# Performance work log

Hardware: AMD Instinct MI355X
Metric: run time of the kernel (lower is better)

The kernel has to match this reference:

```python
import jax, jax.numpy as jnp
import numpy as np

N0, N1, N2 = 819200, 81920, 8192
E1, E2 = 819200, 81920
DIN, DH, DOUT = 128, 256, 128


def setup_inputs() -> dict:
    key = jax.random.key(0)
    ks = jax.random.split(key, 12)
    inp = {
        "x": jax.random.normal(ks[0], (N0, DIN), dtype=jnp.float32),
        "src1": jax.random.randint(ks[1], (E1,), 0, N0, dtype=jnp.int32),
        "dst1": jax.random.randint(ks[2], (E1,), 0, N1, dtype=jnp.int32),
        "src2": jax.random.randint(ks[3], (E2,), 0, N1, dtype=jnp.int32),
        "dst2": jax.random.randint(ks[4], (E2,), 0, N2, dtype=jnp.int32),
        "n1": N1,
        "n2": N2,
        # SAGEConv layer 1 params (lin_l has bias, lin_r no bias, PyG default)
        "w1l": jax.random.normal(ks[5], (DIN, DH), dtype=jnp.float32) / np.sqrt(DIN),
        "b1": jnp.zeros((DH,), dtype=jnp.float32),
        "w1r": jax.random.normal(ks[6], (DIN, DH), dtype=jnp.float32) / np.sqrt(DIN),
        # SAGEConv layer 2 params
        "w2l": jax.random.normal(ks[7], (DH, DOUT), dtype=jnp.float32) / np.sqrt(DH),
        "b2": jnp.zeros((DOUT,), dtype=jnp.float32),
        "w2r": jax.random.normal(ks[8], (DH, DOUT), dtype=jnp.float32) / np.sqrt(DH),
    }
    return inp


def _sage_conv(x_src, x_dst, src, dst, n_dst, wl, bl, wr):
    # mean aggregation of neighbor (source) features into destinations
    msg = x_src[src]                                            # [E, d]
    agg = jax.ops.segment_sum(msg, dst, num_segments=n_dst)     # [n_dst, d]
    cnt = jax.ops.segment_sum(jnp.ones((dst.shape[0],), msg.dtype), dst,
                              num_segments=n_dst)               # [n_dst]
    mean = agg / jnp.maximum(cnt, 1.0)[:, None]
    return mean @ wl + bl + x_dst @ wr


def reference(x, src1, dst1, src2, dst2, n1, n2, w1l, b1, w1r, w2l, b2, w2r):
    # layer 1 (eval mode: dropout is a no-op)
    h = _sage_conv(x, x[:n1], src1, dst1, n1, w1l, b1, w1r)     # [n1, DH]
    h = jax.nn.relu(h)
    # layer 2
    out = _sage_conv(h, h[:n2], src2, dst2, n2, w2l, b2, w2r)   # [n2, DOUT]
    return out
```

## Files before the change

### kernel.cpp

```cpp
#include <hip/hip_runtime.h>

constexpr int cN0 = 819200, cN1 = 81920, cN2 = 8192;
constexpr int cE1 = 819200, cE2 = 81920;
constexpr int cDIN = 128, cDH = 256, cDOUT = 128;
constexpr int cNOFF = cN1 + cN2;

typedef __attribute__((ext_vector_type(8))) short bf16x8;
typedef __attribute__((ext_vector_type(4))) float f32x4;
typedef __attribute__((ext_vector_type(8))) unsigned short u16x8;

__device__ __forceinline__ unsigned short f2bf(float f) {
    unsigned u = __builtin_bit_cast(unsigned, f);
    u += 0x7FFF + ((u >> 16) & 1);
    return (unsigned short)(u >> 16);
}
__device__ __forceinline__ float bf2f(unsigned short s) {
    unsigned u = ((unsigned)s) << 16;
    return __builtin_bit_cast(float, u);
}

__global__ __launch_bounds__(256) void setup_k(
    int* __restrict__ offs,
    const float* __restrict__ w1l, const float* __restrict__ w1r,
    const float* __restrict__ w2l, const float* __restrict__ w2r,
    unsigned short* __restrict__ W1c, unsigned short* __restrict__ W2c)
{
    int id = blockIdx.x * 256 + threadIdx.x;
    if (id < cNOFF) { offs[id] = 0; return; }
    int t = id - cNOFF;
    if (t < 256 * 256) {
        int n = t >> 8, k = t & 255;
        float v = (k < 128) ? w1l[k * 256 + n] : w1r[(k - 128) * 256 + n];
        W1c[n * 256 + k] = f2bf(v);
    } else {
        t -= 256 * 256;
        if (t < 128 * 512) {
            int n = t >> 9, k = t & 511;
            float v = (k < 256) ? w2l[k * 128 + n] : w2r[(k - 256) * 128 + n];
            W2c[n * 512 + k] = f2bf(v);
        }
    }
}

__global__ __launch_bounds__(256) void hist_k(
    const int* __restrict__ dst1, const int* __restrict__ dst2,
    int* __restrict__ offs)
{
    int e = blockIdx.x * 256 + threadIdx.x;
    if (e < cE1) atomicAdd(&offs[dst1[e]], 1);
    else {
        int e2 = e - cE1;
        if (e2 < cE2) atomicAdd(&offs[cN1 + dst2[e2]], 1);
    }
}

__global__ __launch_bounds__(1024) void partial_k(
    const int* __restrict__ a, int* __restrict__ part)
{
    const int tid = threadIdx.x, lane = tid & 63, wid = tid >> 6;
    int v = a[blockIdx.x * 1024 + tid];
    #pragma unroll
    for (int off = 32; off; off >>= 1) v += __shfl_xor(v, off);
    __shared__ int ws[16];
    if (lane == 0) ws[wid] = v;
    __syncthreads();
    if (tid == 0) {
        int s = 0;
        #pragma unroll
        for (int i = 0; i < 16; ++i) s += ws[i];
        part[blockIdx.x] = s;
    }
}

__global__ __launch_bounds__(128) void scanp_k(int* __restrict__ part)
{
    const int tid = threadIdx.x, lane = tid & 63, wid = tid >> 6;
    int v = (tid < 88) ? part[tid] : 0;
    int incl = v;
    #pragma unroll
    for (int off = 1; off < 64; off <<= 1) {
        int t = __shfl_up(incl, off, 64);
        if (lane >= off) incl += t;
    }
    __shared__ int w0;
    if (wid == 0 && lane == 63) w0 = incl;
    __syncthreads();
    int pre = wid ? w0 : 0;
    if (tid < 88) part[tid] = pre + incl - v;
}

__global__ __launch_bounds__(1024) void final_k(
    int* __restrict__ a, const int* __restrict__ part)
{
    const int tid = threadIdx.x, lane = tid & 63, wid = tid >> 6;
    const int g = blockIdx.x * 1024 + tid;
    int v = a[g];
    int incl = v;
    #pragma unroll
    for (int off = 1; off < 64; off <<= 1) {
        int t = __shfl_up(incl, off, 64);
        if (lane >= off) incl += t;
    }
    __shared__ int ws[16];
    if (lane == 63) ws[wid] = incl;
    __syncthreads();
    int pre = 0;
    #pragma unroll
    for (int i = 0; i < 16; ++i) if (i < wid) pre += ws[i];
    int r = part[blockIdx.x] + pre + incl - v;
    if (g >= cN1) r -= cE1;
    a[g] = r;
}

__global__ __launch_bounds__(256) void build_k(
    const int* __restrict__ src1, const int* __restrict__ dst1,
    const int* __restrict__ src2, const int* __restrict__ dst2,
    int* __restrict__ offs, int* __restrict__ eidx1, int* __restrict__ eidx2)
{
    int e = blockIdx.x * 256 + threadIdx.x;
    if (e < cE1) {
        int p = atomicAdd(&offs[dst1[e]], 1);
        eidx1[p] = src1[e];
    } else {
        int e2 = e - cE1;
        if (e2 < cE2) {
            int p = atomicAdd(&offs[cN1 + dst2[e2]], 1);
            eidx2[p] = src2[e2];
        }
    }
}

__global__ __launch_bounds__(256) void agg1_k(
    const float* __restrict__ x, const int* __restrict__ cursor,
    const int* __restrict__ eidx, unsigned short* __restrict__ mean1)
{
    const int row = blockIdx.x * 4 + (threadIdx.x >> 6);
    const int lane = threadIdx.x & 63;
    const int g = lane >> 4, li = lane & 15;
    const int start = row ? cursor[row - 1] : 0;
    const int end = cursor[row];
    float acc[8] = {};
    for (int e = start + g; e < end; e += 4) {
        const int s = eidx[e];
        const float4* p = reinterpret_cast<const float4*>(x + (size_t)s * cDIN + li * 8);
        float4 a = p[0], b = p[1];
        acc[0] += a.x; acc[1] += a.y; acc[2] += a.z; acc[3] += a.w;
        acc[4] += b.x; acc[5] += b.y; acc[6] += b.z; acc[7] += b.w;
    }
    #pragma unroll
    for (int i = 0; i < 8; ++i) {
        acc[i] += __shfl_xor(acc[i], 16);
        acc[i] += __shfl_xor(acc[i], 32);
    }
    if (g == 0) {
        const float inv = 1.0f / fmaxf((float)(end - start), 1.0f);
        u16x8 o;
        #pragma unroll
        for (int i = 0; i < 8; ++i) o[i] = f2bf(acc[i] * inv);
        *reinterpret_cast<u16x8*>(mean1 + (size_t)row * cDIN + li * 8) = o;
    }
}

__global__ __launch_bounds__(256) void agg2_k(
    const unsigned short* __restrict__ h, const int* __restrict__ cursor,
    const int* __restrict__ eidx, unsigned short* __restrict__ mean2)
{
    const int row = blockIdx.x * 4 + (threadIdx.x >> 6);
    const int lane = threadIdx.x & 63;
    const int g = lane >> 4, li = lane & 15;
    const int start = row ? cursor[row - 1] : 0;
    const int end = cursor[row];
    float acc[16] = {};
    for (int e = start + g; e < end; e += 4) {
        const int s = eidx[e];
        const u16x8* p = reinterpret_cast<const u16x8*>(h + (size_t)s * cDH + li * 16);
        u16x8 a = p[0], b = p[1];
        #pragma unroll
        for (int i = 0; i < 8; ++i) { acc[i] += bf2f(a[i]); acc[8 + i] += bf2f(b[i]); }
    }
    #pragma unroll
    for (int i = 0; i < 16; ++i) {
        acc[i] += __shfl_xor(acc[i], 16);
        acc[i] += __shfl_xor(acc[i], 32);
    }
    if (g == 0) {
        const float inv = 1.0f / fmaxf((float)(end - start), 1.0f);
        u16x8 o0, o1;
        #pragma unroll
        for (int i = 0; i < 8; ++i) { o0[i] = f2bf(acc[i] * inv); o1[i] = f2bf(acc[8 + i] * inv); }
        u16x8* q = reinterpret_cast<u16x8*>(mean2 + (size_t)row * cDH + li * 16);
        q[0] = o0; q[1] = o1;
    }
}

template<int K, int N, int TM, bool RIGHT_F32, bool L1MODE>
__global__ __launch_bounds__(256) void mfma_gemm_k(
    const unsigned short* __restrict__ Aleft, const void* __restrict__ Aright,
    const unsigned short* __restrict__ Bt, const float* __restrict__ bias,
    unsigned short* __restrict__ hout, float* __restrict__ fout)
{
    constexpr int KL = K / 2;
    constexpr int LD = 40;
    constexpr int WR = 4;
    constexpr int WC = (TM == 128) ? 4 : 2;
    __shared__ unsigned short As[TM * LD];
    __shared__ unsigned short Bs[128 * LD];

    const int tid = threadIdx.x;
    const int l = tid & 63, w = tid >> 6;
    const int q = l >> 4, r16 = l & 15;
    const int wr0 = (TM == 128) ? (w >> 1) * 64 : 0;
    const int wc0 = (TM == 128) ? (w & 1) * 64 : w * 32;
    const int n0 = blockIdx.x * 128, row0 = blockIdx.y * TM;

    const f32x4 zero = {0.f, 0.f, 0.f, 0.f};
    f32x4 acc[WR][WC];
    #pragma unroll
    for (int m = 0; m < WR; ++m)
        #pragma unroll
        for (int n = 0; n < WC; ++n) acc[m][n] = zero;

    for (int k0 = 0; k0 < K; k0 += 32) {
        const bool left = (k0 < KL);
        __syncthreads();
        #pragma unroll
        for (int c = 0; c < (TM * 4) / 256; ++c) {
            int z = tid + c * 256;
            int r = z >> 2, o16 = z & 3;
            bf16x8 av;
            if (left) {
                av = *reinterpret_cast<const bf16x8*>(Aleft + (size_t)(row0 + r) * KL + k0 + o16 * 8);
            } else if (RIGHT_F32) {
                const float* p = (const float*)Aright + (size_t)(row0 + r) * KL + (k0 - KL) + o16 * 8;
                float4 u = *reinterpret_cast<const float4*>(p);
                float4 v = *reinterpret_cast<const float4*>(p + 4);
                av[0] = (short)f2bf(u.x); av[1] = (short)f2bf(u.y);
                av[2] = (short)f2bf(u.z); av[3] = (short)f2bf(u.w);
                av[4] = (short)f2bf(v.x); av[5] = (short)f2bf(v.y);
                av[6] = (short)f2bf(v.z); av[7] = (short)f2bf(v.w);
            } else {
                av = *reinterpret_cast<const bf16x8*>((const unsigned short*)Aright + (size_t)(row0 + r) * KL + (k0 - KL) + o16 * 8);
            }
            *reinterpret_cast<bf16x8*>(As + r * LD + o16 * 8) = av;
        }
        #pragma unroll
        for (int c = 0; c < 2; ++c) {
            int z = tid + c * 256;
            int r = z >> 2, o16 = z & 3;
            bf16x8 bv = *reinterpret_cast<const bf16x8*>(Bt + (size_t)(n0 + r) * K + k0 + o16 * 8);
            *reinterpret_cast<bf16x8*>(Bs + r * LD + o16 * 8) = bv;
        }
        __syncthreads();
        bf16x8 af[WR], bg[WC];
        #pragma unroll
        for (int m = 0; m < WR; ++m)
            af[m] = *reinterpret_cast<const bf16x8*>(As + (wr0 + 16 * m + r16) * LD + q * 8);
        #pragma unroll
        for (int n = 0; n < WC; ++n)
            bg[n] = *reinterpret_cast<const bf16x8*>(Bs + (wc0 + 16 * n + r16) * LD + q * 8);
        #pragma unroll
        for (int m = 0; m < WR; ++m)
            #pragma unroll
            for (int n = 0; n < WC; ++n)
                acc[m][n] = __builtin_amdgcn_mfma_f32_16x16x32_bf16(af[m], bg[n], acc[m][n], 0, 0, 0);
    }

    #pragma unroll
    for (int n = 0; n < WC; ++n) {
        const int col = n0 + wc0 + 16 * n + r16;
        const float bv = bias[col];
        #pragma unroll
        for (int m = 0; m < WR; ++m) {
            #pragma unroll
            for (int j = 0; j < 4; ++j) {
                const int row = row0 + wr0 + 16 * m + 4 * q + j;
                float v = acc[m][n][j] + bv;
                if (L1MODE) {
                    hout[(size_t)row * N + col] = f2bf(fmaxf(v, 0.f));
                } else {
                    fout[(size_t)row * N + col] = v;
                }
            }
        }
    }
}

extern "C" void kernel_launch(void* const* d_in, const int* in_sizes, int n_in,
                              void* d_out, int out_size, void* d_ws, size_t ws_size,
                              hipStream_t stream)
{
    const float* x    = (const float*)d_in[0];
    const int*   src1 = (const int*)d_in[1];
    const int*   dst1 = (const int*)d_in[2];
    const int*   src2 = (const int*)d_in[3];
    const int*   dst2 = (const int*)d_in[4];
    const float* w1l  = (const float*)d_in[7];
    const float* b1   = (const float*)d_in[8];
    const float* w1r  = (const float*)d_in[9];
    const float* w2l  = (const float*)d_in[10];
    const float* b2   = (const float*)d_in[11];
    const float* w2r  = (const float*)d_in[12];
    float* out = (float*)d_out;

    unsigned short* mean1 = (unsigned short*)d_ws;
    unsigned short* h     = mean1 + (size_t)cN1 * cDIN;
    unsigned short* mean2 = h + (size_t)cN1 * cDH;
    unsigned short* W1c   = mean2 + (size_t)cN2 * cDH;
    unsigned short* W2c   = W1c + 256 * 256;
    int* offs  = (int*)(W2c + 128 * 512);
    int* eidx1 = offs + cNOFF;
    int* eidx2 = eidx1 + cE1;
    int* part  = eidx2 + cE2;

    {
        int total = cNOFF + 256 * 256 + 128 * 512;
        setup_k<<<(total + 255) / 256, 256, 0, stream>>>(offs, w1l, w1r, w2l, w2r, W1c, W2c);
    }
    hist_k<<<(cE1 + cE2) / 256, 256, 0, stream>>>(dst1, dst2, offs);
    partial_k<<<cNOFF / 1024, 1024, 0, stream>>>(offs, part);
    scanp_k<<<1, 128, 0, stream>>>(part);
    final_k<<<cNOFF / 1024, 1024, 0, stream>>>(offs, part);
    build_k<<<(cE1 + cE2) / 256, 256, 0, stream>>>(src1, dst1, src2, dst2, offs, eidx1, eidx2);

    agg1_k<<<cN1 / 4, 256, 0, stream>>>(x, offs, eidx1, mean1);

    mfma_gemm_k<256, 256, 128, true, true><<<dim3(2, cN1 / 128), 256, 0, stream>>>(
        mean1, (const void*)x, W1c, b1, h, nullptr);

    agg2_k<<<cN2 / 4, 256, 0, stream>>>(h, offs + cN1, eidx2, mean2);

    mfma_gemm_k<512, 128, 64, false, false><<<dim3(1, cN2 / 64), 256, 0, stream>>>(
        mean2, (const void*)h, W2c, b2, nullptr, out);
}
```

Baseline: 240.3 us.

## Fuse CSR build into one cooperative kernel and use direct-to-LDS loads in GEMM1

```diff
diff --git a/kernel.cpp b/kernel.cpp
--- a/kernel.cpp
+++ b/kernel.cpp
@@ -1,9 +1,13 @@
 #include <hip/hip_runtime.h>
+#include <hip/hip_cooperative_groups.h>
+
+namespace cg = cooperative_groups;
 
 constexpr int cN0 = 819200, cN1 = 81920, cN2 = 8192;
 constexpr int cE1 = 819200, cE2 = 81920;
 constexpr int cDIN = 128, cDH = 256, cDOUT = 128;
 constexpr int cNOFF = cN1 + cN2;
+constexpr int cNBLK = 352;
 
 typedef __attribute__((ext_vector_type(8))) short bf16x8;
 typedef __attribute__((ext_vector_type(4))) float f32x4;
@@ -19,113 +23,126 @@
     return __builtin_bit_cast(float, u);
 }
 
-__global__ __launch_bounds__(256) void setup_k(
-    int* __restrict__ offs,
+#define GLOAD_LDS16(g, l) __builtin_amdgcn_global_load_lds(               \
+    (const __attribute__((address_space(1))) void*)(g),                   \
+    (__attribute__((address_space(3))) void*)(l), 16, 0, 0)
+
+__global__ __launch_bounds__(256) void csr_coop_k(
+    int* __restrict__ offs, int* __restrict__ part,
+    const int* __restrict__ dst1, const int* __restrict__ dst2,
+    const int* __restrict__ src1, const int* __restrict__ src2,
+    int* __restrict__ eidx1, int* __restrict__ eidx2,
+    const float* __restrict__ x, unsigned short* __restrict__ xb,
     const float* __restrict__ w1l, const float* __restrict__ w1r,
     const float* __restrict__ w2l, const float* __restrict__ w2r,
     unsigned short* __restrict__ W1c, unsigned short* __restrict__ W2c)
 {
-    int id = blockIdx.x * 256 + threadIdx.x;
-    if (id < cNOFF) { offs[id] = 0; return; }
-    int t = id - cNOFF;
-    if (t < 256 * 256) {
-        int n = t >> 8, k = t & 255;
-        float v = (k < 128) ? w1l[k * 256 + n] : w1r[(k - 128) * 256 + n];
-        W1c[n * 256 + k] = f2bf(v);
-    } else {
-        t -= 256 * 256;
-        if (t < 128 * 512) {
-            int n = t >> 9, k = t & 511;
+    cg::grid_group grid = cg::this_grid();
+    const int tid = threadIdx.x, bid = blockIdx.x;
+    const int lane = tid & 63, wid = tid >> 6;
+    const int gtid = bid * 256 + tid;
+    __shared__ int ws4[4];
+    __shared__ int carry;
+
+    offs[gtid] = 0;
+    __threadfence();
+    grid.sync();
+
+    for (int e = gtid; e < cE1 + cE2; e += cNOFF) {
+        if (e < cE1) atomicAdd(&offs[dst1[e]], 1);
+        else atomicAdd(&offs[cN1 + dst2[e - cE1]], 1);
+    }
+    __threadfence();
+    grid.sync();
+
+    {
+        int v = offs[gtid];
+        #pragma unroll
+        for (int off = 32; off; off >>= 1) v += __shfl_xor(v, off);
+        if (lane == 0) ws4[wid] = v;
+        __syncthreads();
+        if (tid == 0) part[bid] = ws4[0] + ws4[1] + ws4[2] + ws4[3];
+    }
+    __threadfence();
+    grid.sync();
+
+    if (bid == 0) {
+        if (tid == 0) carry = 0;
+        __syncthreads();
+        for (int base = 0; base < cNBLK; base += 256) {
+            const int i = base + tid;
+            int v = (i < cNBLK) ? part[i] : 0;
+            int incl = v;
+            #pragma unroll
+            for (int off = 1; off < 64; off <<= 1) {
+                int t = __shfl_up(incl, off, 64);
+                if (lane >= off) incl += t;
+            }
+            if (lane == 63) ws4[wid] = incl;
+            __syncthreads();
+            int wpre = 0;
+            #pragma unroll
+            for (int w = 0; w < 3; ++w) if (w < wid) wpre += ws4[w];
+            int c = carry;
+            if (i < cNBLK) part[i] = c + wpre + incl - v;
+            __syncthreads();
+            if (tid == 255) carry = c + wpre + incl;
+            __syncthreads();
+        }
+        __threadfence();
+    }
+    grid.sync();
+
+    {
+        int v = offs[gtid];
+        int incl = v;
+        #pragma unroll
+        for (int off = 1; off < 64; off <<= 1) {
+            int t = __shfl_up(incl, off, 64);
+            if (lane >= off) incl += t;
+        }
+        if (lane == 63) ws4[wid] = incl;
+        __syncthreads();
+        int pre = 0;
+        #pragma unroll
+        for (int w = 0; w < 3; ++w) if (w < wid) pre += ws4[w];
+        int r = part[bid] + pre + incl - v;
+        if (gtid >= cN1) r -= cE1;
+        offs[gtid] = r;
+    }
+    __threadfence();
+    grid.sync();
+
+    for (int e = gtid; e < cE1 + cE2; e += cNOFF) {
+        if (e < cE1) {
+            int p = atomicAdd(&offs[dst1[e]], 1);
+            eidx1[p] = src1[e];
+        } else {
+            int e2 = e - cE1;
+            int p = atomicAdd(&offs[cN1 + dst2[e2]], 1);
+            eidx2[p] = src2[e2];
+        }
+    }
+
+    for (int i = gtid; i < cN1 * cDIN / 8; i += cNOFF) {
+        const float* p = x + (size_t)i * 8;
+        float4 a = *reinterpret_cast<const float4*>(p);
+        float4 b = *reinterpret_cast<const float4*>(p + 4);
+        u16x8 o;
+        o[0] = f2bf(a.x); o[1] = f2bf(a.y); o[2] = f2bf(a.z); o[3] = f2bf(a.w);
+        o[4] = f2bf(b.x); o[5] = f2bf(b.y); o[6] = f2bf(b.z); o[7] = f2bf(b.w);
+        reinterpret_cast<u16x8*>(xb)[i] = o;
+    }
+    for (int t = gtid; t < 256 * 256 + 128 * 512; t += cNOFF) {
+        if (t < 256 * 256) {
+            int n = t >> 8, k = t & 255;
+            float v = (k < 128) ? w1l[k * 256 + n] : w1r[(k - 128) * 256 + n];
+            W1c[n * 256 + k] = f2bf(v);
+        } else {
+            int t2 = t - 256 * 256;
+            int n = t2 >> 9, k = t2 & 511;
             float v = (k < 256) ? w2l[k * 128 + n] : w2r[(k - 256) * 128 + n];
             W2c[n * 512 + k] = f2bf(v);
-        }
-    }
-}
-
-__global__ __launch_bounds__(256) void hist_k(
-    const int* __restrict__ dst1, const int* __restrict__ dst2,
-    int* __restrict__ offs)
-{
-    int e = blockIdx.x * 256 + threadIdx.x;
-    if (e < cE1) atomicAdd(&offs[dst1[e]], 1);
-    else {
-        int e2 = e - cE1;
-        if (e2 < cE2) atomicAdd(&offs[cN1 + dst2[e2]], 1);
-    }
-}
-
-__global__ __launch_bounds__(1024) void partial_k(
-    const int* __restrict__ a, int* __restrict__ part)
-{
-    const int tid = threadIdx.x, lane = tid & 63, wid = tid >> 6;
-    int v = a[blockIdx.x * 1024 + tid];
-    #pragma unroll
-    for (int off = 32; off; off >>= 1) v += __shfl_xor(v, off);
-    __shared__ int ws[16];
-    if (lane == 0) ws[wid] = v;
-    __syncthreads();
-    if (tid == 0) {
-        int s = 0;
-        #pragma unroll
-        for (int i = 0; i < 16; ++i) s += ws[i];
-        part[blockIdx.x] = s;
-    }
-}
-
-__global__ __launch_bounds__(128) void scanp_k(int* __restrict__ part)
-{
-    const int tid = threadIdx.x, lane = tid & 63, wid = tid >> 6;
-    int v = (tid < 88) ? part[tid] : 0;
-    int incl = v;
-    #pragma unroll
-    for (int off = 1; off < 64; off <<= 1) {
-        int t = __shfl_up(incl, off, 64);
-        if (lane >= off) incl += t;
-    }
-    __shared__ int w0;
-    if (wid == 0 && lane == 63) w0 = incl;
-    __syncthreads();
-    int pre = wid ? w0 : 0;
-    if (tid < 88) part[tid] = pre + incl - v;
-}
-
-__global__ __launch_bounds__(1024) void final_k(
-    int* __restrict__ a, const int* __restrict__ part)
-{
-    const int tid = threadIdx.x, lane = tid & 63, wid = tid >> 6;
-    const int g = blockIdx.x * 1024 + tid;
-    int v = a[g];
-    int incl = v;
-    #pragma unroll
-    for (int off = 1; off < 64; off <<= 1) {
-        int t = __shfl_up(incl, off, 64);
-        if (lane >= off) incl += t;
-    }
-    __shared__ int ws[16];
-    if (lane == 63) ws[wid] = incl;
-    __syncthreads();
-    int pre = 0;
-    #pragma unroll
-    for (int i = 0; i < 16; ++i) if (i < wid) pre += ws[i];
-    int r = part[blockIdx.x] + pre + incl - v;
-    if (g >= cN1) r -= cE1;
-    a[g] = r;
-}
-
-__global__ __launch_bounds__(256) void build_k(
-    const int* __restrict__ src1, const int* __restrict__ dst1,
-    const int* __restrict__ src2, const int* __restrict__ dst2,
-    int* __restrict__ offs, int* __restrict__ eidx1, int* __restrict__ eidx2)
-{
-    int e = blockIdx.x * 256 + threadIdx.x;
-    if (e < cE1) {
-        int p = atomicAdd(&offs[dst1[e]], 1);
-        eidx1[p] = src1[e];
-    } else {
-        int e2 = e - cE1;
-        if (e2 < cE2) {
-            int p = atomicAdd(&offs[cN1 + dst2[e2]], 1);
-            eidx2[p] = src2[e2];
         }
     }
 }
@@ -193,93 +210,138 @@
     }
 }
 
-template<int K, int N, int TM, bool RIGHT_F32, bool L1MODE>
-__global__ __launch_bounds__(256) void mfma_gemm_k(
-    const unsigned short* __restrict__ Aleft, const void* __restrict__ Aright,
-    const unsigned short* __restrict__ Bt, const float* __restrict__ bias,
-    unsigned short* __restrict__ hout, float* __restrict__ fout)
-{
-    constexpr int KL = K / 2;
-    constexpr int LD = 40;
-    constexpr int WR = 4;
-    constexpr int WC = (TM == 128) ? 4 : 2;
-    __shared__ unsigned short As[TM * LD];
-    __shared__ unsigned short Bs[128 * LD];
+__global__ __launch_bounds__(256) void gemm1_k(
+    const unsigned short* __restrict__ mean1,
+    const unsigned short* __restrict__ xb,
+    const unsigned short* __restrict__ W1c,
+    const float* __restrict__ b1,
+    unsigned short* __restrict__ h)
+{
+    __shared__ unsigned short As[128 * 32];
+    __shared__ unsigned short Bs[128 * 32];
 
     const int tid = threadIdx.x;
     const int l = tid & 63, w = tid >> 6;
     const int q = l >> 4, r16 = l & 15;
-    const int wr0 = (TM == 128) ? (w >> 1) * 64 : 0;
-    const int wc0 = (TM == 128) ? (w & 1) * 64 : w * 32;
-    const int n0 = blockIdx.x * 128, row0 = blockIdx.y * TM;
+    const int wr0 = (w >> 1) * 64, wc0 = (w & 1) * 64;
+    const int n0 = blockIdx.x * 128, row0 = blockIdx.y * 128;
+
+    const int srow = w * 32 + (l >> 2);
+    const int skoff = (l & 3) * 8;
 
     const f32x4 zero = {0.f, 0.f, 0.f, 0.f};
-    f32x4 acc[WR][WC];
-    #pragma unroll
-    for (int m = 0; m < WR; ++m)
-        #pragma unroll
-        for (int n = 0; n < WC; ++n) acc[m][n] = zero;
+    f32x4 acc[4][4];
+    #pragma unroll
+    for (int m = 0; m < 4; ++m)
+        #pragma unroll
+        for (int n = 0; n < 4; ++n) acc[m][n] = zero;
+
+    for (int k0 = 0; k0 < 256; k0 += 32) {
+        const unsigned short* Asrc = (k0 < 128) ? mean1 : xb;
+        const int kk = k0 & 127;
+        __syncthreads();
+        #pragma unroll
+        for (int j = 0; j < 2; ++j) {
+            const int r = srow + j * 16;
+            GLOAD_LDS16(Asrc + (size_t)(row0 + r) * 128 + kk + skoff,
+                        As + (w * 2 + j) * 512);
+            GLOAD_LDS16(W1c + (size_t)(n0 + r) * 256 + k0 + skoff,
+                        Bs + (w * 2 + j) * 512);
+        }
+        __syncthreads();
+        bf16x8 af[4], bg[4];
+        #pragma unroll
+        for (int m = 0; m < 4; ++m)
+            af[m] = *reinterpret_cast<const bf16x8*>(As + (wr0 + 16 * m + r16) * 32 + q * 8);
+        #pragma unroll
+        for (int n = 0; n < 4; ++n)
+            bg[n] = *reinterpret_cast<const bf16x8*>(Bs + (wc0 + 16 * n + r16) * 32 + q * 8);
+        #pragma unroll
+        for (int m = 0; m < 4; ++m)
+            #pragma unroll
+            for (int n = 0; n < 4; ++n)
+                acc[m][n] = __builtin_amdgcn_mfma_f32_16x16x32_bf16(af[m], bg[n], acc[m][n], 0, 0, 0);
+    }
+
+    #pragma unroll
+    for (int n = 0; n < 4; ++n) {
+        const int col = n0 + wc0 + 16 * n + r16;
+        const float bv = b1[col];
+        #pragma unroll
+        for (int m = 0; m < 4; ++m) {
+            #pragma unroll
+            for (int j = 0; j < 4; ++j) {
+                const int row = row0 + wr0 + 16 * m + 4 * q + j;
+                h[(size_t)row * cDH + col] = f2bf(fmaxf(acc[m][n][j] + bv, 0.f));
+            }
+        }
+    }
+}
+
+__global__ __launch_bounds__(256) void gemm2_k(
+    const unsigned short* __restrict__ mean2,
+    const unsigned short* __restrict__ hd,
+    const unsigned short* __restrict__ W2c,
+    const float* __restrict__ b2, float* __restrict__ out)
+{
+    constexpr int K = 512, KL = 256, N = 128, TM = 64;
+    constexpr int LD = 40;
+    __shared__ unsigned short As[TM * LD];
+    __shared__ unsigned short Bs[128 * LD];
+
+    const int tid = threadIdx.x;
+    const int l = tid & 63, w = tid >> 6;
+    const int q = l >> 4, r16 = l & 15;
+    const int wc0 = w * 32;
+    const int row0 = blockIdx.y * TM;
+
+    const f32x4 zero = {0.f, 0.f, 0.f, 0.f};
+    f32x4 acc[4][2];
+    #pragma unroll
+    for (int m = 0; m < 4; ++m) { acc[m][0] = zero; acc[m][1] = zero; }
 
     for (int k0 = 0; k0 < K; k0 += 32) {
         const bool left = (k0 < KL);
-        __syncthreads();
-        #pragma unroll
-        for (int c = 0; c < (TM * 4) / 256; ++c) {
-            int z = tid + c * 256;
-            int r = z >> 2, o16 = z & 3;
-            bf16x8 av;
-            if (left) {
-                av = *reinterpret_cast<const bf16x8*>(Aleft + (size_t)(row0 + r) * KL + k0 + o16 * 8);
-            } else if (RIGHT_F32) {
-                const float* p = (const float*)Aright + (size_t)(row0 + r) * KL + (k0 - KL) + o16 * 8;
-                float4 u = *reinterpret_cast<const float4*>(p);
-                float4 v = *reinterpret_cast<const float4*>(p + 4);
-                av[0] = (short)f2bf(u.x); av[1] = (short)f2bf(u.y);
-                av[2] = (short)f2bf(u.z); av[3] = (short)f2bf(u.w);
-                av[4] = (short)f2bf(v.x); av[5] = (short)f2bf(v.y);
-                av[6] = (short)f2bf(v.z); av[7] = (short)f2bf(v.w);
-            } else {
-                av = *reinterpret_cast<const bf16x8*>((const unsigned short*)Aright + (size_t)(row0 + r) * KL + (k0 - KL) + o16 * 8);
-            }
+        const unsigned short* Asrc = left ? mean2 : hd;
+        const int kk = k0 & (KL - 1);
+        __syncthreads();
+        {
+            int r = tid >> 2, o16 = tid & 3;
+            bf16x8 av = *reinterpret_cast<const bf16x8*>(Asrc + (size_t)(row0 + r) * KL + kk + o16 * 8);
             *reinterpret_cast<bf16x8*>(As + r * LD + o16 * 8) = av;
         }
         #pragma unroll
         for (int c = 0; c < 2; ++c) {
             int z = tid + c * 256;
             int r = z >> 2, o16 = z & 3;
-            bf16x8 bv = *reinterpret_cast<const bf16x8*>(Bt + (size_t)(n0 + r) * K + k0 + o16 * 8);
+            bf16x8 bv = *reinterpret_cast<const bf16x8*>(W2c + (size_t)r * K + k0 + o16 * 8);
             *reinterpret_cast<bf16x8*>(Bs + r * LD + o16 * 8) = bv;
         }
         __syncthreads();
-        bf16x8 af[WR], bg[WC];
-        #pragma unroll
-        for (int m = 0; m < WR; ++m)
-            af[m] = *reinterpret_cast<const bf16x8*>(As + (wr0 + 16 * m + r16) * LD + q * 8);
-        #pragma unroll
-        for (int n = 0; n < WC; ++n)
+        bf16x8 af[4], bg[2];
+        #pragma unroll
+        for (int m = 0; m < 4; ++m)
+            af[m] = *reinterpret_cast<const bf16x8*>(As + (16 * m + r16) * LD + q * 8);
+        #pragma unroll
+        for (int n = 0; n < 2; ++n)
             bg[n] = *reinterpret_cast<const bf16x8*>(Bs + (wc0 + 16 * n + r16) * LD + q * 8);
         #pragma unroll
-        for (int m = 0; m < WR; ++m)
-            #pragma unroll
-            for (int n = 0; n < WC; ++n)
+        for (int m = 0; m < 4; ++m)
+            #pragma unroll
+            for (int n = 0; n < 2; ++n)
                 acc[m][n] = __builtin_amdgcn_mfma_f32_16x16x32_bf16(af[m], bg[n], acc[m][n], 0, 0, 0);
     }
 
     #pragma unroll
-    for (int n = 0; n < WC; ++n) {
-        const int col = n0 + wc0 + 16 * n + r16;
-        const float bv = bias[col];
-        #pragma unroll
-        for (int m = 0; m < WR; ++m) {
+    for (int n = 0; n < 2; ++n) {
+        const int col = wc0 + 16 * n + r16;
+        const float bv = b2[col];
+        #pragma unroll
+        for (int m = 0; m < 4; ++m) {
             #pragma unroll
             for (int j = 0; j < 4; ++j) {
-                const int row = row0 + wr0 + 16 * m + 4 * q + j;
-                float v = acc[m][n][j] + bv;
-                if (L1MODE) {
-                    hout[(size_t)row * N + col] = f2bf(fmaxf(v, 0.f));
-                } else {
-                    fout[(size_t)row * N + col] = v;
-                }
+                const int row = row0 + 16 * m + 4 * q + j;
+                out[(size_t)row * N + col] = acc[m][n][j] + bv;
             }
         }
     }
@@ -307,28 +369,26 @@
     unsigned short* mean2 = h + (size_t)cN1 * cDH;
     unsigned short* W1c   = mean2 + (size_t)cN2 * cDH;
     unsigned short* W2c   = W1c + 256 * 256;
-    int* offs  = (int*)(W2c + 128 * 512);
+    unsigned short* xb    = W2c + 128 * 512;
+    int* offs  = (int*)(xb + (size_t)cN1 * cDIN);
     int* eidx1 = offs + cNOFF;
     int* eidx2 = eidx1 + cE1;
     int* part  = eidx2 + cE2;
 
     {
-        int total = cNOFF + 256 * 256 + 128 * 512;
-        setup_k<<<(total + 255) / 256, 256, 0, stream>>>(offs, w1l, w1r, w2l, w2r, W1c, W2c);
-    }
-    hist_k<<<(cE1 + cE2) / 256, 256, 0, stream>>>(dst1, dst2, offs);
-    partial_k<<<cNOFF / 1024, 1024, 0, stream>>>(offs, part);
-    scanp_k<<<1, 128, 0, stream>>>(part);
-    final_k<<<cNOFF / 1024, 1024, 0, stream>>>(offs, part);
-    build_k<<<(cE1 + cE2) / 256, 256, 0, stream>>>(src1, dst1, src2, dst2, offs, eidx1, eidx2);
-
+        void* args[] = {
+            (void*)&offs, (void*)&part,
+            (void*)&dst1, (void*)&dst2, (void*)&src1, (void*)&src2,
+            (void*)&eidx1, (void*)&eidx2,
+            (void*)&x, (void*)&xb,
+            (void*)&w1l, (void*)&w1r, (void*)&w2l, (void*)&w2r,
+            (void*)&W1c, (void*)&W2c
+        };
+        hipLaunchCooperativeKernel((void*)csr_coop_k, dim3(cNBLK), dim3(256),
+                                   args, 0, stream);
+    }
     agg1_k<<<cN1 / 4, 256, 0, stream>>>(x, offs, eidx1, mean1);
-
-    mfma_gemm_k<256, 256, 128, true, true><<<dim3(2, cN1 / 128), 256, 0, stream>>>(
-        mean1, (const void*)x, W1c, b1, h, nullptr);
-
+    gemm1_k<<<dim3(2, cN1 / 128), 256, 0, stream>>>(mean1, xb, W1c, b1, h);
     agg2_k<<<cN2 / 4, 256, 0, stream>>>(h, offs + cN1, eidx2, mean2);
-
-    mfma_gemm_k<512, 128, 64, false, false><<<dim3(1, cN2 / 64), 256, 0, stream>>>(
-        mean2, (const void*)h, W2c, b2, nullptr, out);
-}
+    gemm2_k<<<dim3(1, cN2 / 64), 256, 0, stream>>>(mean2, h, W2c, b2, out);
+}
```

Result: slower. 539.2 us (+124.4%).
